# Kernel optimization log

Measured on AMD Instinct MI355X. Metric: run time of the kernel, lower is better.

The kernel has to match this reference:

```python
import jax, jax.numpy as jnp
import numpy as np

B, S, D = 8, 4096, 1024

def setup_inputs() -> dict:
    key = jax.random.key(0)
    ks = jax.random.split(key, 5)
    scale = 1.0 / np.sqrt(D)
    x = jax.random.normal(ks[0], (B, S, D), dtype=jnp.float32)
    Wq = jax.random.normal(ks[1], (D, D), dtype=jnp.float32) * scale
    Wk = jax.random.normal(ks[2], (D, D), dtype=jnp.float32) * scale
    Wv = jax.random.normal(ks[3], (D, D), dtype=jnp.float32) * scale
    Wp = jax.random.normal(ks[4], (D, D), dtype=jnp.float32) * scale
    bp = jnp.zeros((D,), dtype=jnp.float32)
    return {"x": x, "Wq": Wq, "Wk": Wk, "Wv": Wv, "Wp": Wp, "bp": bp}

def reference(x, Wq, Wk, Wv, Wp, bp):
    # torch nn.Linear(no bias): y = x @ W^T
    q = jnp.einsum('bsd,ed->bse', x, Wq)
    k = jnp.einsum('bsd,ed->bse', x, Wk)
    v = jnp.einsum('bsd,ed->bse', x, Wv)
    # Linear attention (no softmax): (Q K^T) V == Q (K^T V), use associative order
    kv = jnp.einsum('bse,bsf->bef', k, v)       # [B, D, D]
    z = jnp.einsum('bse,bef->bsf', q, kv)       # [B, S, D]
    out = jnp.einsum('bsf,gf->bsg', z, Wp) + bp + x
    return out
```

## Files before the change

### kernel.cpp

```cpp
#include <hip/hip_runtime.h>
#include <hip/hip_bf16.h>


#define B_DIM 8
#define S_DIM 4096
#define D_DIM 1024
#define M_TOT (B_DIM * S_DIM)

using short8 = __attribute__((ext_vector_type(8))) short;
using f32x4  = __attribute__((ext_vector_type(4))) float;

#define TILE_M 128
#define TILE_N 128
#define TILE_K 64

__device__ __forceinline__ void g2l16(const void* g, void* l) {
  __builtin_amdgcn_global_load_lds(
      (const __attribute__((address_space(1))) unsigned int*)g,
      (__attribute__((address_space(3))) unsigned int*)l, 16, 0, 0);
}

__device__ __forceinline__ unsigned short f2b(float f) {
  __hip_bfloat16 h = __float2bfloat16(f);
  return __builtin_bit_cast(unsigned short, h);
}

__device__ __forceinline__ float b2f(unsigned short u) {
  return __bfloat162float(__builtin_bit_cast(__hip_bfloat16, u));
}

template<bool FINAL, bool SYMM>
__global__ __launch_bounds__(256, 3)
void gemm_bt(const unsigned short* __restrict__ A,
             const unsigned short* __restrict__ Bt,
             void* __restrict__ C,
             int K, int lda, int ldb, int ldc,
             long long sA, long long sB, long long sC,
             const float* __restrict__ bias)
{
  __shared__ __align__(16) unsigned short smem[TILE_M * TILE_K + TILE_N * TILE_K];
  unsigned short* As = smem;
  unsigned short* Bs = smem + TILE_M * TILE_K;

  const int tid  = threadIdx.x;
  const int wave = tid >> 6;
  const int lane = tid & 63;
  const int qd   = lane >> 4;
  const int ln   = lane & 15;
  const int wr   = (wave >> 1) * 64;
  const int wc   = (wave & 1) * 64;

  int bx, by;
  if constexpr (SYMM) {
    int r = blockIdx.x, row = 0;
    while (r >= 8 - row) { r -= 8 - row; ++row; }
    by = row; bx = row + r;
  } else {
    const int flat = blockIdx.y * gridDim.x + blockIdx.x;
    const int strp = flat & 7;
    const int t8   = flat >> 3;
    bx = t8 % gridDim.x;
    by = strp * (gridDim.y >> 3) + t8 / gridDim.x;
  }

  const long long m0 = (long long)by * TILE_M;
  const long long n0 = (long long)bx * TILE_N;
  const int bz = blockIdx.z;

  const unsigned short* Ab = A  + (long long)bz * sA;
  const unsigned short* Bb = Bt + (long long)bz * sB;

  const int srow = tid >> 3;
  const int scg  = ((tid & 7) + (tid >> 3)) & 7;
  const unsigned short* pA = Ab + (m0 + srow) * lda + scg * 8;
  const unsigned short* pB = Bb + (n0 + srow) * ldb + scg * 8;
  const long long rsA = 32LL * lda, rsB = 32LL * ldb;
  unsigned short* lA = As + wave * 512;
  unsigned short* lB = Bs + wave * 512;

  int rowA[4], sA0[4], rowB[4], sB0[4];
#pragma unroll
  for (int i = 0; i < 4; ++i) {
    int ra = wr + i * 16 + ln;
    int rb = wc + i * 16 + ln;
    rowA[i] = ra * 64;  sA0[i] = (qd - ra) & 7;
    rowB[i] = rb * 64;  sB0[i] = (qd - rb) & 7;
  }

  f32x4 acc[4][4];
#pragma unroll
  for (int i = 0; i < 4; ++i)
#pragma unroll
    for (int j = 0; j < 4; ++j)
      acc[i][j] = (f32x4){0.f, 0.f, 0.f, 0.f};

  for (int k0 = 0; k0 < K; k0 += TILE_K) {
#pragma unroll
    for (int it = 0; it < 4; ++it) g2l16(pA + it * rsA, lA + it * 2048);
#pragma unroll
    for (int it = 0; it < 4; ++it) g2l16(pB + it * rsB, lB + it * 2048);
    __syncthreads();

#pragma unroll
    for (int kk = 0; kk < 2; ++kk) {
      short8 af[4], bf[4];
#pragma unroll
      for (int i = 0; i < 4; ++i)
        af[i] = *(const short8*)(As + rowA[i] + (((sA0[i] + kk * 4) & 7) << 3));
#pragma unroll
      for (int j = 0; j < 4; ++j)
        bf[j] = *(const short8*)(Bs + rowB[j] + (((sB0[j] + kk * 4) & 7) << 3));
#pragma unroll
      for (int i = 0; i < 4; ++i)
#pragma unroll
        for (int j = 0; j < 4; ++j)
          acc[i][j] = __builtin_amdgcn_mfma_f32_16x16x32_bf16(af[i], bf[j], acc[i][j], 0, 0, 0);
    }
    __syncthreads();
    pA += TILE_K; pB += TILE_K;
  }

  float* Ct = (float*)smem;
  const int fr = tid >> 3;
  const int fc = (tid & 7) * 4;
  const int hr = tid >> 4;
  const int hc = (tid & 15) * 4;

#pragma unroll
  for (int p = 0; p < 4; ++p) {
    __syncthreads();
    if ((wr >> 6) == (p >> 1)) {
      const int ibase = (p & 1) * 2;
#pragma unroll
      for (int ii = 0; ii < 2; ++ii)
#pragma unroll
        for (int j = 0; j < 4; ++j)
#pragma unroll
          for (int r = 0; r < 4; ++r)
            Ct[(ii * 16 + qd * 4 + r) * 132 + wc + j * 16 + ln] = acc[ibase + ii][j][r];
    }
    __syncthreads();

    if constexpr (FINAL) {
      float* Cf = (float*)C + (long long)bz * sC;
      const long long grow = m0 + p * 32 + fr;
#pragma unroll
      for (int s = 0; s < 4; ++s) {
        const int c = fc + s * 32;
        float4 v = *(const float4*)(Ct + fr * 132 + c);
        const float4 bb = *(const float4*)(bias + n0 + c);
        v.x += bb.x; v.y += bb.y; v.z += bb.z; v.w += bb.w;
        *(float4*)(Cf + grow * ldc + n0 + c) = v;
      }
    } else {
      unsigned short* Cb = (unsigned short*)C + (long long)bz * sC;
#pragma unroll
      for (int rs = 0; rs < 2; ++rs) {
        const int row = hr + rs * 16;
        const long long grow = m0 + p * 32 + row;
#pragma unroll
        for (int s = 0; s < 2; ++s) {
          const int c = hc + s * 64;
          float4 v = *(const float4*)(Ct + row * 132 + c);
          ushort4 u;
          u.x = f2b(v.x); u.y = f2b(v.y); u.z = f2b(v.z); u.w = f2b(v.w);
          *(ushort4*)(Cb + grow * ldc + n0 + c) = u;
        }
      }
    }
  }
}

__global__ __launch_bounds__(256)
void mirror_sym(unsigned short* __restrict__ G)
{
  __shared__ unsigned short tile[64][68];
  int p = blockIdx.x, i = 1;
  while (p >= i) { p -= i; ++i; }
  const int j = p;
  const int dr0 = i * 128 + (blockIdx.y >> 1) * 64;
  const int dc0 = j * 128 + (blockIdx.y & 1) * 64;
  unsigned short* Gb = G + (size_t)blockIdx.z * D_DIM * D_DIM;
  const int tx = threadIdx.x & 15;
  const int ty = threadIdx.x >> 4;

#pragma unroll
  for (int r = 0; r < 4; ++r) {
    int row = ty * 4 + r;
    ushort4 d = *(const ushort4*)(Gb + (size_t)(dc0 + row) * D_DIM + dr0 + tx * 4);
    *(ushort4*)&tile[row][tx * 4] = d;
  }
  __syncthreads();
#pragma unroll
  for (int r = 0; r < 4; ++r) {
    int row = ty * 4 + r;
    ushort4 d;
    d.x = tile[tx * 4 + 0][row];
    d.y = tile[tx * 4 + 1][row];
    d.z = tile[tx * 4 + 2][row];
    d.w = tile[tx * 4 + 3][row];
    *(ushort4*)(Gb + (size_t)(dr0 + row) * D_DIM + dc0 + tx * 4) = d;
  }
}

__global__ __launch_bounds__(256)
void add_eye(unsigned short* __restrict__ ET)
{
  const int d = blockIdx.x * 256 + threadIdx.x;
  const size_t idx = (size_t)blockIdx.y * D_DIM * D_DIM + (size_t)d * D_DIM + d;
  ET[idx] = f2b(b2f(ET[idx]) + 1.0f);
}

__global__ __launch_bounds__(256)
void cast_transpose_x(const float* __restrict__ x,
                      unsigned short* __restrict__ xb,
                      unsigned short* __restrict__ xT)
{
  __shared__ unsigned short tile[64][68];
  const int b  = blockIdx.z;
  const int s0 = blockIdx.x * 64;
  const int e0 = blockIdx.y * 64;
  const int tx = threadIdx.x & 15;
  const int ty = threadIdx.x >> 4;

#pragma unroll
  for (int r = 0; r < 4; ++r) {
    int s = ty * 4 + r;
    const size_t off = ((size_t)b * S_DIM + s0 + s) * D_DIM + e0 + tx * 4;
    float4 f = *(const float4*)(x + off);
    ushort4 u;
    u.x = f2b(f.x); u.y = f2b(f.y); u.z = f2b(f.z); u.w = f2b(f.w);
    *(ushort4*)&tile[s][tx * 4] = u;
    *(ushort4*)(xb + off) = u;
  }
  __syncthreads();
#pragma unroll
  for (int r = 0; r < 4; ++r) {
    int e = ty * 4 + r;
    ushort4 d;
    d.x = tile[tx * 4 + 0][e];
    d.y = tile[tx * 4 + 1][e];
    d.z = tile[tx * 4 + 2][e];
    d.w = tile[tx * 4 + 3][e];
    *(ushort4*)(xT + ((size_t)b * D_DIM + e0 + e) * S_DIM + s0 + tx * 4) = d;
  }
}

__global__ __launch_bounds__(256)
void cast_transpose_w(const float* __restrict__ Wq, const float* __restrict__ Wk,
                      const float* __restrict__ Wv,
                      unsigned short* __restrict__ WqT, unsigned short* __restrict__ WkT,
                      unsigned short* __restrict__ WvT)
{
  __shared__ unsigned short tile[64][68];
  const int z = blockIdx.z;
  const float* src = (z == 0) ? Wq : (z == 1) ? Wk : Wv;
  unsigned short* dst = (z == 0) ? WqT : (z == 1) ? WkT : WvT;
  const int e0 = blockIdx.x * 64;
  const int d0 = blockIdx.y * 64;
  const int tx = threadIdx.x & 15;
  const int ty = threadIdx.x >> 4;

#pragma unroll
  for (int r = 0; r < 4; ++r) {
    int e = ty * 4 + r;
    float4 f = *(const float4*)(src + (size_t)(e0 + e) * D_DIM + d0 + tx * 4);
    ushort4 u;
    u.x = f2b(f.x); u.y = f2b(f.y); u.z = f2b(f.z); u.w = f2b(f.w);
    *(ushort4*)&tile[e][tx * 4] = u;
  }
  __syncthreads();
#pragma unroll
  for (int r = 0; r < 4; ++r) {
    int d = ty * 4 + r;
    ushort4 o;
    o.x = tile[tx * 4 + 0][d];
    o.y = tile[tx * 4 + 1][d];
    o.z = tile[tx * 4 + 2][d];
    o.w = tile[tx * 4 + 3][d];
    *(ushort4*)(dst + (size_t)(d0 + d) * D_DIM + e0 + tx * 4) = o;
  }
}

__global__ __launch_bounds__(256)
void cast_f32_bf16(const float* __restrict__ src, unsigned short* __restrict__ dst, int n4)
{
  int i = blockIdx.x * 256 + threadIdx.x;
  if (i >= n4) return;
  float4 f = ((const float4*)src)[i];
  ushort4 u;
  u.x = f2b(f.x); u.y = f2b(f.y); u.z = f2b(f.z); u.w = f2b(f.w);
  ((ushort4*)dst)[i] = u;
}

extern "C" void kernel_launch(void* const* d_in, const int* in_sizes, int n_in,
                              void* d_out, int out_size, void* d_ws, size_t ws_size,
                              hipStream_t stream) {
  const float* x  = (const float*)d_in[0];
  const float* Wq = (const float*)d_in[1];
  const float* Wk = (const float*)d_in[2];
  const float* Wv = (const float*)d_in[3];
  const float* Wp = (const float*)d_in[4];
  const float* bp = (const float*)d_in[5];
  float* out = (float*)d_out;
  char* ws = (char*)d_ws;

  unsigned short* xb   = (unsigned short*)(ws + 0);
  unsigned short* Wpb  = (unsigned short*)(ws + 67108864);
  unsigned short* WqTb = (unsigned short*)(ws + 69206016);
  unsigned short* WvTb = (unsigned short*)(ws + 71303168);
  unsigned short* WkTb = (unsigned short*)(ws + 73400320);
  unsigned short* P1   = (unsigned short*)(ws + 75497472);
  unsigned short* P2T  = (unsigned short*)(ws + 77594624);
  unsigned short* xT   = (unsigned short*)(ws + 79691776);
  unsigned short* G    = (unsigned short*)(ws + 146800640);
  unsigned short* T    = (unsigned short*)(ws + 163577856);
  unsigned short* ET   = (unsigned short*)(ws + 180355072);

  const long long DD = (long long)D_DIM * D_DIM;
  const long long SD = (long long)S_DIM * D_DIM;

  dim3 gx(S_DIM / 64, D_DIM / 64, B_DIM);
  cast_transpose_x<<<gx, 256, 0, stream>>>(x, xb, xT);

  cast_f32_bf16<<<dim3(D_DIM * D_DIM / 4 / 256), 256, 0, stream>>>(Wp, Wpb, D_DIM * D_DIM / 4);
  cast_transpose_w<<<dim3(16, 16, 3), 256, 0, stream>>>(Wq, Wk, Wv, WqTb, WkTb, WvTb);

  dim3 gw(D_DIM / TILE_N, D_DIM / TILE_M, 2);
  gemm_bt<false, false><<<gw, 256, 0, stream>>>(Wpb, WvTb, P1, D_DIM, D_DIM, D_DIM, D_DIM,
                                                DD, DD, DD, nullptr);

  gemm_bt<false, true><<<dim3(36, 1, B_DIM), 256, 0, stream>>>(
      xT, xT, G, S_DIM, S_DIM, S_DIM, D_DIM, SD, SD, DD, nullptr);
  mirror_sym<<<dim3(28, 4, B_DIM), 256, 0, stream>>>(G);

  dim3 g1k(D_DIM / TILE_N, D_DIM / TILE_M, B_DIM);
  gemm_bt<false, false><<<g1k, 256, 0, stream>>>(P1, G, T, D_DIM, D_DIM, D_DIM, D_DIM,
                                                 0, DD, DD, nullptr);

  gemm_bt<false, false><<<g1k, 256, 0, stream>>>(T, P2T, ET, D_DIM, D_DIM, D_DIM, D_DIM,
                                                 DD, 0, DD, nullptr);

  add_eye<<<dim3(D_DIM / 256, B_DIM), 256, 0, stream>>>(ET);

  dim3 gf(D_DIM / TILE_N, S_DIM / TILE_M, B_DIM);
  gemm_bt<true, false><<<gf, 256, 0, stream>>>(xb, ET, out, D_DIM, D_DIM, D_DIM, D_DIM,
                                               SD, DD, SD, bp);
  (void)in_sizes; (void)n_in; (void)out_size; (void)ws_size;
}
```

Measured before the change: 493.4 us.

## Fuse symmetric mirror and identity add into GEMM epilogues, merge weight prep

The symmetric Gram GEMM now writes the transposed copy of each off-diagonal tile directly from the shared-memory staging buffer, which removes the separate mirror kernel. The identity add is folded into the epilogue of the ET GEMM through a new template flag, and the Wp cast is merged into the weight-transpose kernel. Launch bounds rise from 3 to 4 waves per SIMD. Together these cut three launches and a global re-read of G, at the cost of strided shared-memory reads in the mirror path and possible register pressure.

```diff
diff --git a/kernel.cpp b/kernel.cpp
--- a/kernel.cpp
+++ b/kernel.cpp
@@ -25,12 +25,8 @@
   return __builtin_bit_cast(unsigned short, h);
 }
 
-__device__ __forceinline__ float b2f(unsigned short u) {
-  return __bfloat162float(__builtin_bit_cast(__hip_bfloat16, u));
-}
-
-template<bool FINAL, bool SYMM>
-__global__ __launch_bounds__(256, 3)
+template<bool FINAL, bool SYMM, bool ADDI>
+__global__ __launch_bounds__(256, 4)
 void gemm_bt(const unsigned short* __restrict__ A,
              const unsigned short* __restrict__ Bt,
              void* __restrict__ C,
@@ -162,53 +158,37 @@
         for (int s = 0; s < 2; ++s) {
           const int c = hc + s * 64;
           float4 v = *(const float4*)(Ct + row * 132 + c);
+          if constexpr (ADDI) {
+            const int dj = (int)(grow - (n0 + c));
+            if (dj == 0) v.x += 1.0f;
+            else if (dj == 1) v.y += 1.0f;
+            else if (dj == 2) v.z += 1.0f;
+            else if (dj == 3) v.w += 1.0f;
+          }
           ushort4 u;
           u.x = f2b(v.x); u.y = f2b(v.y); u.z = f2b(v.z); u.w = f2b(v.w);
           *(ushort4*)(Cb + grow * ldc + n0 + c) = u;
         }
       }
+      if constexpr (SYMM) {
+        if (m0 != n0) {
+          const int mr = tid >> 1;
+          const int mc = (tid & 1) * 16;
+          const long long trow = n0 + mr;
+          const long long tcol = m0 + p * 32 + mc;
+#pragma unroll
+          for (int jj = 0; jj < 4; ++jj) {
+            ushort4 u;
+            u.x = f2b(Ct[(mc + jj * 4 + 0) * 132 + mr]);
+            u.y = f2b(Ct[(mc + jj * 4 + 1) * 132 + mr]);
+            u.z = f2b(Ct[(mc + jj * 4 + 2) * 132 + mr]);
+            u.w = f2b(Ct[(mc + jj * 4 + 3) * 132 + mr]);
+            *(ushort4*)(Cb + trow * ldc + tcol + jj * 4) = u;
+          }
+        }
+      }
     }
   }
-}
-
-__global__ __launch_bounds__(256)
-void mirror_sym(unsigned short* __restrict__ G)
-{
-  __shared__ unsigned short tile[64][68];
-  int p = blockIdx.x, i = 1;
-  while (p >= i) { p -= i; ++i; }
-  const int j = p;
-  const int dr0 = i * 128 + (blockIdx.y >> 1) * 64;
-  const int dc0 = j * 128 + (blockIdx.y & 1) * 64;
-  unsigned short* Gb = G + (size_t)blockIdx.z * D_DIM * D_DIM;
-  const int tx = threadIdx.x & 15;
-  const int ty = threadIdx.x >> 4;
-
-#pragma unroll
-  for (int r = 0; r < 4; ++r) {
-    int row = ty * 4 + r;
-    ushort4 d = *(const ushort4*)(Gb + (size_t)(dc0 + row) * D_DIM + dr0 + tx * 4);
-    *(ushort4*)&tile[row][tx * 4] = d;
-  }
-  __syncthreads();
-#pragma unroll
-  for (int r = 0; r < 4; ++r) {
-    int row = ty * 4 + r;
-    ushort4 d;
-    d.x = tile[tx * 4 + 0][row];
-    d.y = tile[tx * 4 + 1][row];
-    d.z = tile[tx * 4 + 2][row];
-    d.w = tile[tx * 4 + 3][row];
-    *(ushort4*)(Gb + (size_t)(dr0 + row) * D_DIM + dc0 + tx * 4) = d;
-  }
-}
-
-__global__ __launch_bounds__(256)
-void add_eye(unsigned short* __restrict__ ET)
-{
-  const int d = blockIdx.x * 256 + threadIdx.x;
-  const size_t idx = (size_t)blockIdx.y * D_DIM * D_DIM + (size_t)d * D_DIM + d;
-  ET[idx] = f2b(b2f(ET[idx]) + 1.0f);
 }
 
 __global__ __launch_bounds__(256)
@@ -247,19 +227,33 @@
 }
 
 __global__ __launch_bounds__(256)
-void cast_transpose_w(const float* __restrict__ Wq, const float* __restrict__ Wk,
-                      const float* __restrict__ Wv,
-                      unsigned short* __restrict__ WqT, unsigned short* __restrict__ WkT,
-                      unsigned short* __restrict__ WvT)
+void prep_w(const float* __restrict__ Wq, const float* __restrict__ Wk,
+            const float* __restrict__ Wv, const float* __restrict__ Wp,
+            unsigned short* __restrict__ WqT, unsigned short* __restrict__ WkT,
+            unsigned short* __restrict__ WvT, unsigned short* __restrict__ Wpb)
 {
   __shared__ unsigned short tile[64][68];
   const int z = blockIdx.z;
-  const float* src = (z == 0) ? Wq : (z == 1) ? Wk : Wv;
-  unsigned short* dst = (z == 0) ? WqT : (z == 1) ? WkT : WvT;
   const int e0 = blockIdx.x * 64;
   const int d0 = blockIdx.y * 64;
   const int tx = threadIdx.x & 15;
   const int ty = threadIdx.x >> 4;
+
+  if (z == 3) {
+#pragma unroll
+    for (int r = 0; r < 4; ++r) {
+      int e = ty * 4 + r;
+      const size_t off = (size_t)(e0 + e) * D_DIM + d0 + tx * 4;
+      float4 f = *(const float4*)(Wp + off);
+      ushort4 u;
+      u.x = f2b(f.x); u.y = f2b(f.y); u.z = f2b(f.z); u.w = f2b(f.w);
+      *(ushort4*)(Wpb + off) = u;
+    }
+    return;
+  }
+
+  const float* src = (z == 0) ? Wq : (z == 1) ? Wk : Wv;
+  unsigned short* dst = (z == 0) ? WqT : (z == 1) ? WkT : WvT;
 
 #pragma unroll
   for (int r = 0; r < 4; ++r) {
@@ -280,17 +274,6 @@
     o.w = tile[tx * 4 + 3][d];
     *(ushort4*)(dst + (size_t)(d0 + d) * D_DIM + e0 + tx * 4) = o;
   }
-}
-
-__global__ __launch_bounds__(256)
-void cast_f32_bf16(const float* __restrict__ src, unsigned short* __restrict__ dst, int n4)
-{
-  int i = blockIdx.x * 256 + threadIdx.x;
-  if (i >= n4) return;
-  float4 f = ((const float4*)src)[i];
-  ushort4 u;
-  u.x = f2b(f.x); u.y = f2b(f.y); u.z = f2b(f.z); u.w = f2b(f.w);
-  ((ushort4*)dst)[i] = u;
 }
 
 extern "C" void kernel_launch(void* const* d_in, const int* in_sizes, int n_in,
@@ -323,28 +306,24 @@
   dim3 gx(S_DIM / 64, D_DIM / 64, B_DIM);
   cast_transpose_x<<<gx, 256, 0, stream>>>(x, xb, xT);
 
-  cast_f32_bf16<<<dim3(D_DIM * D_DIM / 4 / 256), 256, 0, stream>>>(Wp, Wpb, D_DIM * D_DIM / 4);
-  cast_transpose_w<<<dim3(16, 16, 3), 256, 0, stream>>>(Wq, Wk, Wv, WqTb, WkTb, WvTb);
+  prep_w<<<dim3(16, 16, 4), 256, 0, stream>>>(Wq, Wk, Wv, Wp, WqTb, WkTb, WvTb, Wpb);
 
   dim3 gw(D_DIM / TILE_N, D_DIM / TILE_M, 2);
-  gemm_bt<false, false><<<gw, 256, 0, stream>>>(Wpb, WvTb, P1, D_DIM, D_DIM, D_DIM, D_DIM,
-                                                DD, DD, DD, nullptr);
-
-  gemm_bt<false, true><<<dim3(36, 1, B_DIM), 256, 0, stream>>>(
+  gemm_bt<false, false, false><<<gw, 256, 0, stream>>>(
+      Wpb, WvTb, P1, D_DIM, D_DIM, D_DIM, D_DIM, DD, DD, DD, nullptr);
+
+  gemm_bt<false, true, false><<<dim3(36, 1, B_DIM), 256, 0, stream>>>(
       xT, xT, G, S_DIM, S_DIM, S_DIM, D_DIM, SD, SD, DD, nullptr);
-  mirror_sym<<<dim3(28, 4, B_DIM), 256, 0, stream>>>(G);
 
   dim3 g1k(D_DIM / TILE_N, D_DIM / TILE_M, B_DIM);
-  gemm_bt<false, false><<<g1k, 256, 0, stream>>>(P1, G, T, D_DIM, D_DIM, D_DIM, D_DIM,
-                                                 0, DD, DD, nullptr);
-
-  gemm_bt<false, false><<<g1k, 256, 0, stream>>>(T, P2T, ET, D_DIM, D_DIM, D_DIM, D_DIM,
-                                                 DD, 0, DD, nullptr);
-
-  add_eye<<<dim3(D_DIM / 256, B_DIM), 256, 0, stream>>>(ET);
+  gemm_bt<false, false, false><<<g1k, 256, 0, stream>>>(
+      P1, G, T, D_DIM, D_DIM, D_DIM, D_DIM, 0, DD, DD, nullptr);
+
+  gemm_bt<false, false, true><<<g1k, 256, 0, stream>>>(
+      T, P2T, ET, D_DIM, D_DIM, D_DIM, D_DIM, DD, 0, DD, nullptr);
 
   dim3 gf(D_DIM / TILE_N, S_DIM / TILE_M, B_DIM);
-  gemm_bt<true, false><<<gf, 256, 0, stream>>>(xb, ET, out, D_DIM, D_DIM, D_DIM, D_DIM,
-                                               SD, DD, SD, bp);
+  gemm_bt<true, false, false><<<gf, 256, 0, stream>>>(
+      xb, ET, out, D_DIM, D_DIM, D_DIM, D_DIM, SD, DD, SD, bp);
   (void)in_sizes; (void)n_in; (void)out_size; (void)ws_size;
 }
```

After: 488.7 us. About the same (-0.9%).
